# Kernel tuning notes

Measured on AMD Instinct MI355X. Metric: run time of the kernel, lower is better.

Reference implementation:

```python
import jax, jax.numpy as jnp
import numpy as np

B, N, DIN, D, E, STEP = 4, 1024, 256, 256, 5, 5


def setup_inputs() -> dict:
    key = jax.random.key(0)
    ks = jax.random.split(key, 14)
    s = 0.02  # weight init scale
    inp = {
        "node_features": jax.random.normal(ks[0], (B, N, DIN), dtype=jnp.float32),
        # dense per-edge-type adjacency; scaled so messages stay in a sane range
        "adj_matrices": jax.random.uniform(ks[1], (B, E, N, N), dtype=jnp.float32) * (2.0 / N),
        "fc_in_w": jax.random.normal(ks[2], (D, DIN), dtype=jnp.float32) * s,
        "fc_in_b": jnp.zeros((D,), dtype=jnp.float32),
        "edge_w": jax.random.normal(ks[3], (E, D, D), dtype=jnp.float32) * s,
        "edge_b": jax.random.normal(ks[4], (E, D), dtype=jnp.float32) * s,
        "gru_w_ih": jax.random.normal(ks[5], (3 * D, D), dtype=jnp.float32) * s,
        "gru_w_hh": jax.random.normal(ks[6], (3 * D, D), dtype=jnp.float32) * s,
        "gru_b_ih": jnp.zeros((3 * D,), dtype=jnp.float32),
        "gru_b_hh": jnp.zeros((3 * D,), dtype=jnp.float32),
        "conv1_w": jax.random.normal(ks[7], (D, D), dtype=jnp.float32) * s,
        "conv1_b": jnp.zeros((D,), dtype=jnp.float32),
        "conv2_w": jax.random.normal(ks[8], (D, D), dtype=jnp.float32) * s,
        "conv2_b": jnp.zeros((D,), dtype=jnp.float32),
    }
    return inp


def _gru_cell(x, h, w_ih, w_hh, b_ih, b_hh):
    # torch GRUCell: gates ordered [r, z, n]
    gi = x @ w_ih.T + b_ih  # [B*N, 3D]
    gh = h @ w_hh.T + b_hh
    ir, iz, inn = jnp.split(gi, 3, axis=-1)
    hr, hz, hn = jnp.split(gh, 3, axis=-1)
    r = jax.nn.sigmoid(ir + hr)
    z = jax.nn.sigmoid(iz + hz)
    n = jnp.tanh(inn + r * hn)
    return (1.0 - z) * n + z * h


def reference(node_features, adj_matrices, fc_in_w, fc_in_b, edge_w, edge_b,
              gru_w_ih, gru_w_hh, gru_b_ih, gru_b_hh,
              conv1_w, conv1_b, conv2_w, conv2_b):
    h = node_features @ fc_in_w.T + fc_in_b  # [B, N, D]
    sum_edge_b = jnp.sum(edge_b, axis=0)  # accumulated biases over edge types
    for _ in range(STEP):
        # messages per edge type: adj_e @ h  -> [B, E, N, D]
        msgs = jnp.einsum('benm,bmd->bend', adj_matrices, h)
        # per-edge-type linear (y = x @ W_e.T) then accumulate over edge types
        acc = jnp.einsum('bend,ekd->bnk', msgs, edge_w) + sum_edge_b  # [B, N, D]
        h = _gru_cell(acc, h, gru_w_ih, gru_w_hh, gru_b_ih, gru_b_hh)
    node_states = h  # [B, N, D]
    # conv1d with kernel_size=1 over node axis == per-node linear on channels
    attn_weights = jax.nn.sigmoid(node_states @ conv1_w.T + conv1_b)  # [B, N, D]
    feats = jnp.tanh(node_states @ conv2_w.T + conv2_b)  # [B, N, D]
    graph_embedding = jnp.sum(attn_weights * feats, axis=1)  # sum over nodes -> [B, D]
    attn_map = jnp.mean(attn_weights, axis=2)  # mean over channels -> [B, N]
    return (graph_embedding, node_states, attn_map)
```

## Files before the change

### kernel.cpp

```cpp
#include <hip/hip_runtime.h>
#include <hip/hip_bf16.h>
#include <cstdint>


typedef __attribute__((ext_vector_type(8))) short bf16x8;
typedef __attribute__((ext_vector_type(4))) float f32x4;

__device__ __forceinline__ float bf2f(__hip_bfloat16 x) { return __bfloat162float(x); }
__device__ __forceinline__ __hip_bfloat16 f2bf(float x) { return __float2bfloat16(x); }
__device__ __forceinline__ short f2bs(float x) {
  __hip_bfloat16 h = __float2bfloat16(x);
  return *reinterpret_cast<short*>(&h);
}
__device__ __forceinline__ float s2f(short x) {
  __hip_bfloat16 h = *reinterpret_cast<__hip_bfloat16*>(&x);
  return __bfloat162float(h);
}

__device__ __forceinline__ bf16x8 ld8_ext(const void* base, long off, bool f32) {
  if (f32) {
    const float* p = (const float*)base + off;
    bf16x8 r;
#pragma unroll
    for (int i = 0; i < 8; ++i) r[i] = f2bs(p[i]);
    return r;
  }
  return *(const bf16x8*)((const __hip_bfloat16*)base + off);
}

__device__ __forceinline__ bf16x8 ld8_sum5(const __hip_bfloat16* part, int row, int k) {
  const long base = (long)row * 256 + (long)(row >> 10) * 1048576 + k;
  float s[8] = {0.f, 0.f, 0.f, 0.f, 0.f, 0.f, 0.f, 0.f};
#pragma unroll
  for (int e = 0; e < 5; ++e) {
    bf16x8 v = *(const bf16x8*)(part + base + e * 262144);
#pragma unroll
    for (int j = 0; j < 8; ++j) s[j] += s2f(v[j]);
  }
  bf16x8 r;
#pragma unroll
  for (int j = 0; j < 8; ++j) r[j] = f2bs(s[j]);
  return r;
}

__device__ __forceinline__ void gload16(const __hip_bfloat16* g, __hip_bfloat16* l) {
  __builtin_amdgcn_global_load_lds(
      (const __attribute__((address_space(1))) void*)g,
      (__attribute__((address_space(3))) void*)l, 16, 0, 0);
}

__global__ void detect_dtype(const uint32_t* __restrict__ raw, int* __restrict__ flag) {
  __shared__ int cnt;
  if (threadIdx.x == 0) cnt = 0;
  __syncthreads();
  int c = 0;
  for (int i = threadIdx.x; i < 512; i += 256) {
    uint32_t byte = (raw[i] >> 8) & 0xFF;
    if (byte >= 0x28 && byte <= 0x40) ++c;
  }
  atomicAdd(&cnt, c);
  __syncthreads();
  if (threadIdx.x == 0) *flag = (cnt < 300) ? 1 : 0;
}

__global__ void prep_pool(const void* fcb, const void* bih, const void* bhh,
                          const void* c1b, const void* c2b, const void* edgeb,
                          const int* __restrict__ flag,
                          float* __restrict__ pool, float* __restrict__ ge,
                          float* __restrict__ am32) {
  const bool f32 = (*flag != 0);
  for (int t = threadIdx.x; t < 2560; t += 256) {
    const void* p; int i;
    if (t < 256)       { p = fcb;  i = t; }
    else if (t < 1024) { p = bih;  i = t - 256; }
    else if (t < 1792) { p = bhh;  i = t - 1024; }
    else if (t < 2048) { p = c1b;  i = t - 1792; }
    else if (t < 2304) { p = c2b;  i = t - 2048; }
    else {
      int k = t - 2304; float s = 0.f;
      for (int e = 0; e < 5; ++e)
        s += f32 ? ((const float*)edgeb)[e * 256 + k]
                 : bf2f(((const __hip_bfloat16*)edgeb)[e * 256 + k]);
      pool[t] = s; continue;
    }
    pool[t] = f32 ? ((const float*)p)[i] : bf2f(((const __hip_bfloat16*)p)[i]);
  }
  for (int t = threadIdx.x; t < 1024; t += 256) ge[t] = 0.f;
  for (int t = threadIdx.x; t < 4096; t += 256) am32[t] = 0.f;
}

__global__ void bias_gi_k(const float* __restrict__ pool,
                          const __hip_bfloat16* __restrict__ wih,
                          float* __restrict__ out) {
  const int n = blockIdx.x * 256 + threadIdx.x;
  if (n >= 768) return;
  float s = pool[256 + n];
  for (int k = 0; k < 256; ++k) s += pool[2304 + k] * bf2f(wih[n * 256 + k]);
  out[n] = s;
}

__global__ void wcvt_all(const void* fcw, const void* edw, const void* wih,
                         const void* whh, const void* c1w, const void* c2w,
                         const int* __restrict__ flag, __hip_bfloat16* __restrict__ dst) {
  const bool f32 = (*flag != 0);
  const int i = blockIdx.x * 256 + threadIdx.x;
  const void* src; int off;
  if      (i < 65536)  { src = fcw; off = i; }
  else if (i < 393216) { src = edw; off = i - 65536; }
  else if (i < 589824) { src = wih; off = i - 393216; }
  else if (i < 786432) { src = whh; off = i - 589824; }
  else if (i < 851968) { src = c1w; off = i - 786432; }
  else                 { src = c2w; off = i - 851968; }
  dst[i] = f32 ? f2bf(((const float*)src)[off])
               : ((const __hip_bfloat16*)src)[off];
}

__global__ void adj_cvt(const void* __restrict__ src, const int* __restrict__ flag,
                        __hip_bfloat16* __restrict__ dst) {
  const bool f32 = (*flag != 0);
  const long i = ((long)blockIdx.x * 256 + threadIdx.x) * 8;
  bf16x8 r;
  if (f32) {
    const float* p = (const float*)src + i;
#pragma unroll
    for (int j = 0; j < 8; ++j) r[j] = f2bs(p[j]);
  } else {
    r = *(const bf16x8*)((const __hip_bfloat16*)src + i);
  }
  *(bf16x8*)(dst + i) = r;
}

__global__ void sum_part(const __hip_bfloat16* __restrict__ part,
                         __hip_bfloat16* __restrict__ out) {
  const int t = blockIdx.x * 256 + threadIdx.x;
  const int row = t >> 5;
  const int k = (t & 31) * 8;
  const long base = (long)row * 256 + (long)(row >> 10) * 1048576 + k;
  float s[8] = {0.f, 0.f, 0.f, 0.f, 0.f, 0.f, 0.f, 0.f};
#pragma unroll
  for (int e = 0; e < 5; ++e) {
    bf16x8 v = *(const bf16x8*)(part + base + e * 262144);
#pragma unroll
    for (int j = 0; j < 8; ++j) s[j] += s2f(v[j]);
  }
  bf16x8 r;
#pragma unroll
  for (int j = 0; j < 8; ++j) r[j] = f2bs(s[j]);
  *(bf16x8*)(out + (long)row * 256 + k) = r;
}

template<bool HAS_BIAS, bool DUAL>
__global__ __launch_bounds__(256)
void gemm128(const __hip_bfloat16* __restrict__ A, const __hip_bfloat16* __restrict__ Bt,
             const float* __restrict__ bias, __hip_bfloat16* __restrict__ C,
             const __hip_bfloat16* __restrict__ A2, const __hip_bfloat16* __restrict__ Bt2,
             const float* __restrict__ bias2, __hip_bfloat16* __restrict__ C2,
             int K, int lda, int ldb, int ldc,
             long aBatch, int zdivA, int zmodA,
             long bBatch, int zdivB, int zmodB,
             long cBatch, int zdivC, int zSplit)
{
  __shared__ __align__(16) __hip_bfloat16 sA[128 * 64];
  __shared__ __align__(16) __hip_bfloat16 sB[128 * 64];
  const int t = threadIdx.x;
  const int w = t >> 6;
  const int l = t & 63;
  const int m0 = blockIdx.x * 128;
  const int n0 = blockIdx.y * 128;
  int z = blockIdx.z;

  const __hip_bfloat16* Au = A; const __hip_bfloat16* Btu = Bt;
  const float* biasu = bias; __hip_bfloat16* Cu = C;
  if (DUAL && z >= zSplit) { Au = A2; Btu = Bt2; biasu = bias2; Cu = C2; z -= zSplit; }

  const __hip_bfloat16* Ab = Au + (long)((z / zdivA) % zmodA) * aBatch;
  const __hip_bfloat16* Bb = Btu + (long)((z / zdivB) % zmodB) * bBatch;

  const int srow = l >> 3;
  const int scol = (l & 7) * 8;

  f32x4 acc[4][4];
#pragma unroll
  for (int i = 0; i < 4; ++i)
#pragma unroll
    for (int j = 0; j < 4; ++j) acc[i][j] = (f32x4){0.f, 0.f, 0.f, 0.f};

  const int wr = (w >> 1) * 64;
  const int wc = (w & 1) * 64;
  const int r15 = l & 15;
  const int quad = l >> 4;

  for (int k0 = 0; k0 < K; k0 += 64) {
    __syncthreads();
#pragma unroll
    for (int i = 0; i < 4; ++i) {
      const int c = w * 4 + i;
      const int row = c * 8 + srow;
      gload16(Ab + (long)(m0 + row) * lda + (k0 + scol), sA + c * 512);
      gload16(Bb + (long)(n0 + row) * ldb + (k0 + scol), sB + c * 512);
    }
    __syncthreads();
#pragma unroll
    for (int ks = 0; ks < 2; ++ks) {
      const int cg = (ks * 4 + quad) * 8;
      bf16x8 aF[4], bF[4];
#pragma unroll
      for (int i = 0; i < 4; ++i)
        aF[i] = *(const bf16x8*)(sA + (wr + i * 16 + r15) * 64 + cg);
#pragma unroll
      for (int i = 0; i < 4; ++i)
        bF[i] = *(const bf16x8*)(sB + (wc + i * 16 + r15) * 64 + cg);
#pragma unroll
      for (int mi = 0; mi < 4; ++mi)
#pragma unroll
        for (int ni = 0; ni < 4; ++ni)
          acc[mi][ni] = __builtin_amdgcn_mfma_f32_16x16x32_bf16(
              aF[mi], bF[ni], acc[mi][ni], 0, 0, 0);
    }
  }

  const long cOff = (long)(z / zdivC) * cBatch;
#pragma unroll
  for (int mi = 0; mi < 4; ++mi) {
#pragma unroll
    for (int ni = 0; ni < 4; ++ni) {
      const int n = n0 + wc + ni * 16 + r15;
      float bv = 0.f;
      if (HAS_BIAS) bv = biasu[n];
#pragma unroll
      for (int r = 0; r < 4; ++r) {
        const int m = m0 + wr + mi * 16 + quad * 4 + r;
        Cu[cOff + (long)m * ldc + n] = f2bf(acc[mi][ni][r] + bv);
      }
    }
  }
}

template<int OUT_MODE, bool HAS_BIAS, int A_MODE, bool DUAL>
__global__ __launch_bounds__(256)
void gemm_bt(const void* __restrict__ A, const __hip_bfloat16* __restrict__ Bt,
             const float* __restrict__ bias, void* __restrict__ Cp,
             const void* __restrict__ A2, const __hip_bfloat16* __restrict__ Bt2,
             const float* __restrict__ bias2, void* __restrict__ Cp2,
             const int* __restrict__ flag,
             int Kg, int ngrp, int lda, int ldb, int ldc,
             long aBatch, int zdivA, int zmodA,
             long bBatch, int zdivB, int zmodB,
             long cBatch, int zdivC, long aGrp, long bGrp, int zSplit)
{
  __shared__ __align__(16) __hip_bfloat16 sA[64 * 64];
  __shared__ __align__(16) __hip_bfloat16 sB[64 * 64];
  const bool af32 = (A_MODE == 1) ? (*flag != 0) : false;
  const int t = threadIdx.x;
  const int w = t >> 6;
  const int l = t & 63;
  const int m0 = blockIdx.x * 64;
  const int n0 = blockIdx.y * 64;
  int z = blockIdx.z;

  const void* Au = A; const __hip_bfloat16* Btu = Bt;
  const float* biasu = bias; void* Cpu = Cp;
  bool second = false;
  if (DUAL && z >= zSplit) {
    Au = A2; Btu = Bt2; biasu = bias2; Cpu = Cp2; z -= zSplit; second = true;
  }

  const long aOff = (long)((z / zdivA) % zmodA) * aBatch;
  const __hip_bfloat16* Bb = Btu + (long)((z / zdivB) % zmodB) * bBatch;

  const int p0 = t, p1 = t + 256;
  const int sr0 = p0 >> 3, sc0 = (p0 & 7) ^ (sr0 & 7);
  const int sr1 = p1 >> 3, sc1 = (p1 & 7) ^ (sr1 & 7);

  f32x4 acc[4];
#pragma unroll
  for (int i = 0; i < 4; ++i) acc[i] = (f32x4){0.f, 0.f, 0.f, 0.f};

  const int mrow = w * 16 + (l & 15);
  const int quad = l >> 4;

  for (int g = 0; g < ngrp; ++g) {
    const long aG = aOff + (long)g * aGrp;
    const __hip_bfloat16* Bg = Bb + (long)g * bGrp;
    for (int k0 = 0; k0 < Kg; k0 += 64) {
      bf16x8 a0, a1;
      if (A_MODE == 2 && !second) {
        a0 = ld8_sum5((const __hip_bfloat16*)Au, m0 + sr0, k0 + sc0 * 8);
        a1 = ld8_sum5((const __hip_bfloat16*)Au, m0 + sr1, k0 + sc1 * 8);
      } else if (A_MODE == 1) {
        a0 = ld8_ext(Au, aG + (long)(m0 + sr0) * lda + (k0 + sc0 * 8), af32);
        a1 = ld8_ext(Au, aG + (long)(m0 + sr1) * lda + (k0 + sc1 * 8), af32);
      } else {
        const __hip_bfloat16* Ab = (const __hip_bfloat16*)Au;
        a0 = *(const bf16x8*)(Ab + aG + (long)(m0 + sr0) * lda + (k0 + sc0 * 8));
        a1 = *(const bf16x8*)(Ab + aG + (long)(m0 + sr1) * lda + (k0 + sc1 * 8));
      }
      bf16x8 b0 = *(const bf16x8*)(Bg + (long)(n0 + sr0) * ldb + (k0 + sc0 * 8));
      bf16x8 b1 = *(const bf16x8*)(Bg + (long)(n0 + sr1) * ldb + (k0 + sc1 * 8));
      __syncthreads();
      *(bf16x8*)(sA + p0 * 8) = a0;
      *(bf16x8*)(sA + p1 * 8) = a1;
      *(bf16x8*)(sB + p0 * 8) = b0;
      *(bf16x8*)(sB + p1 * 8) = b1;
      __syncthreads();
#pragma unroll
      for (int ks = 0; ks < 2; ++ks) {
        const int cg = ks * 4 + quad;
        bf16x8 af = *(const bf16x8*)(sA + mrow * 64 + ((cg ^ (mrow & 7)) * 8));
#pragma unroll
        for (int t4 = 0; t4 < 4; ++t4) {
          const int nrow = t4 * 16 + (l & 15);
          bf16x8 bfr = *(const bf16x8*)(sB + nrow * 64 + ((cg ^ (nrow & 7)) * 8));
          acc[t4] = __builtin_amdgcn_mfma_f32_16x16x32_bf16(af, bfr, acc[t4], 0, 0, 0);
        }
      }
    }
  }

  const long cOff = (long)(z / zdivC) * cBatch;
#pragma unroll
  for (int t4 = 0; t4 < 4; ++t4) {
    const int n = n0 + t4 * 16 + (l & 15);
    float bv = 0.f;
    if (HAS_BIAS) bv = biasu[n];
#pragma unroll
    for (int r = 0; r < 4; ++r) {
      const int m = m0 + w * 16 + quad * 4 + r;
      const float v = acc[t4][r] + bv;
      if (OUT_MODE == 0)
        ((__hip_bfloat16*)Cpu)[cOff + (long)m * ldc + n] = f2bf(v);
      else
        ((float*)Cpu)[cOff + (long)m * ldc + n] = v;
    }
  }
}

__global__ void gru_gate8(const __hip_bfloat16* __restrict__ gi,
                          const __hip_bfloat16* __restrict__ gh,
                          __hip_bfloat16* __restrict__ hbf,
                          void* __restrict__ ns_out, const int* __restrict__ flag)
{
  const int t = blockIdx.x * 256 + threadIdx.x;
  const int m = t >> 5;
  const int k = (t & 31) * 8;
  const long gb = (long)m * 768 + k;
  bf16x8 vir = *(const bf16x8*)(gi + gb);
  bf16x8 viz = *(const bf16x8*)(gi + gb + 256);
  bf16x8 vin = *(const bf16x8*)(gi + gb + 512);
  bf16x8 vhr = *(const bf16x8*)(gh + gb);
  bf16x8 vhz = *(const bf16x8*)(gh + gb + 256);
  bf16x8 vhn = *(const bf16x8*)(gh + gb + 512);
  const long hidx = (long)m * 256 + k;
  bf16x8 vh = *(const bf16x8*)(hbf + hidx);
  bf16x8 out;
  float hf[8];
#pragma unroll
  for (int j = 0; j < 8; ++j) {
    const float r = 1.f / (1.f + __expf(-(s2f(vir[j]) + s2f(vhr[j]))));
    const float zz = 1.f / (1.f + __expf(-(s2f(viz[j]) + s2f(vhz[j]))));
    const float nn = tanhf(s2f(vin[j]) + r * s2f(vhn[j]));
    hf[j] = (1.f - zz) * nn + zz * s2f(vh[j]);
    out[j] = f2bs(hf[j]);
  }
  *(bf16x8*)(hbf + hidx) = out;
  if (ns_out) {
    if (*flag) {
      float* o = (float*)ns_out + 1024 + hidx;
#pragma unroll
      for (int j = 0; j < 8; ++j) o[j] = hf[j];
    } else {
      *(bf16x8*)((__hip_bfloat16*)ns_out + 1024 + hidx) = out;
    }
  }
}

__global__ __launch_bounds__(256)
void conv_fused(const __hip_bfloat16* __restrict__ hbf,
                const __hip_bfloat16* __restrict__ c1w,
                const __hip_bfloat16* __restrict__ c2w,
                const float* __restrict__ pool,
                float* __restrict__ geg, float* __restrict__ am32)
{
  __shared__ __align__(16) __hip_bfloat16 sA[64 * 64];
  __shared__ __align__(16) __hip_bfloat16 sB1[64 * 64];
  __shared__ __align__(16) __hip_bfloat16 sB2[64 * 64];
  __shared__ float sge[64];
  __shared__ float sam[64];
  const int t = threadIdx.x, w = t >> 6, l = t & 63;
  const int m0 = blockIdx.x * 64, n0 = blockIdx.y * 64;
  if (t < 64) { sge[t] = 0.f; sam[t] = 0.f; }
  const int p0 = t, p1 = t + 256;
  const int sr0 = p0 >> 3, sc0 = (p0 & 7) ^ (sr0 & 7);
  const int sr1 = p1 >> 3, sc1 = (p1 & 7) ^ (sr1 & 7);
  f32x4 a1[4], a2[4];
#pragma unroll
  for (int i = 0; i < 4; ++i) { a1[i] = (f32x4){0,0,0,0}; a2[i] = (f32x4){0,0,0,0}; }
  const int mrow = w * 16 + (l & 15);
  const int quad = l >> 4;
  for (int k0 = 0; k0 < 256; k0 += 64) {
    bf16x8 va0 = *(const bf16x8*)(hbf + (long)(m0 + sr0) * 256 + (k0 + sc0 * 8));
    bf16x8 va1 = *(const bf16x8*)(hbf + (long)(m0 + sr1) * 256 + (k0 + sc1 * 8));
    bf16x8 vb0 = *(const bf16x8*)(c1w + (long)(n0 + sr0) * 256 + (k0 + sc0 * 8));
    bf16x8 vb1 = *(const bf16x8*)(c1w + (long)(n0 + sr1) * 256 + (k0 + sc1 * 8));
    bf16x8 vc0 = *(const bf16x8*)(c2w + (long)(n0 + sr0) * 256 + (k0 + sc0 * 8));
    bf16x8 vc1 = *(const bf16x8*)(c2w + (long)(n0 + sr1) * 256 + (k0 + sc1 * 8));
    __syncthreads();
    *(bf16x8*)(sA + p0 * 8) = va0;  *(bf16x8*)(sA + p1 * 8) = va1;
    *(bf16x8*)(sB1 + p0 * 8) = vb0; *(bf16x8*)(sB1 + p1 * 8) = vb1;
    *(bf16x8*)(sB2 + p0 * 8) = vc0; *(bf16x8*)(sB2 + p1 * 8) = vc1;
    __syncthreads();
#pragma unroll
    for (int ks = 0; ks < 2; ++ks) {
      const int cg = ks * 4 + quad;
      bf16x8 af = *(const bf16x8*)(sA + mrow * 64 + ((cg ^ (mrow & 7)) * 8));
#pragma unroll
      for (int t4 = 0; t4 < 4; ++t4) {
        const int nrow = t4 * 16 + (l & 15);
        bf16x8 b1f = *(const bf16x8*)(sB1 + nrow * 64 + ((cg ^ (nrow & 7)) * 8));
        bf16x8 b2f = *(const bf16x8*)(sB2 + nrow * 64 + ((cg ^ (nrow & 7)) * 8));
        a1[t4] = __builtin_amdgcn_mfma_f32_16x16x32_bf16(af, b1f, a1[t4], 0, 0, 0);
        a2[t4] = __builtin_amdgcn_mfma_f32_16x16x32_bf16(af, b2f, a2[t4], 0, 0, 0);
      }
    }
  }
  float asum[4] = {0.f, 0.f, 0.f, 0.f};
#pragma unroll
  for (int t4 = 0; t4 < 4; ++t4) {
    const int n = n0 + t4 * 16 + (l & 15);
    const float bb1 = pool[1792 + n], bb2 = pool[2048 + n];
    float g = 0.f;
#pragma unroll
    for (int r = 0; r < 4; ++r) {
      const float av = 1.f / (1.f + __expf(-(a1[t4][r] + bb1)));
      const float fv = tanhf(a2[t4][r] + bb2);
      g += av * fv;
      asum[r] += av;
    }
    atomicAdd(&sge[t4 * 16 + (l & 15)], g);
  }
#pragma unroll
  for (int r = 0; r < 4; ++r) atomicAdd(&sam[w * 16 + quad * 4 + r], asum[r]);
  __syncthreads();
  if (t < 64) atomicAdd(&geg[(m0 >> 10) * 256 + n0 + t], sge[t]);
  else if (t < 128) atomicAdd(&am32[m0 + (t - 64)], sam[t - 64]);
}

__global__ void finish_out(const float* __restrict__ ge, const float* __restrict__ am32,
                           void* __restrict__ dout, const int* __restrict__ flag)
{
  const int t = blockIdx.x * 256 + threadIdx.x;
  const bool f32 = (*flag != 0);
  if (t < 1024) {
    if (f32) ((float*)dout)[t] = ge[t];
    else     ((__hip_bfloat16*)dout)[t] = f2bf(ge[t]);
  } else {
    const float v = am32[t - 1024] * (1.f / 256.f);
    if (f32) ((float*)dout)[1049600 + t - 1024] = v;
    else     ((__hip_bfloat16*)dout)[1049600 + t - 1024] = f2bf(v);
  }
}

extern "C" void kernel_launch(void* const* d_in, const int* in_sizes, int n_in,
                              void* d_out, int out_size, void* d_ws, size_t ws_size,
                              hipStream_t stream) {
  (void)in_sizes; (void)n_in; (void)out_size;
  const void* node_f = d_in[0];
  const void* adj    = d_in[1];
  const void* fc_w   = d_in[2];
  const void* fc_b   = d_in[3];
  const void* edge_w = d_in[4];
  const void* edge_b = d_in[5];
  const void* w_ih   = d_in[6];
  const void* w_hh   = d_in[7];
  const void* b_ih   = d_in[8];
  const void* b_hh   = d_in[9];
  const void* c1w    = d_in[10];
  const void* c1b    = d_in[11];
  const void* c2w    = d_in[12];
  const void* c2b    = d_in[13];

  char* ws = (char*)d_ws;
  const size_t MB = (size_t)1 << 20;
  int*            flag = (int*)(ws);
  float*          bp   = (float*)(ws + 256);
  float*          ge   = (float*)(ws + 14336);
  float*          am32 = (float*)(ws + 18432);
  __hip_bfloat16* wbf  = (__hip_bfloat16*)(ws + 34816);
  __hip_bfloat16* hbf  = (__hip_bfloat16*)(ws + 1869824);
  char*           S    = ws + 3966976;
  __hip_bfloat16* heT  = (__hip_bfloat16*)(S);
  __hip_bfloat16* part = (__hip_bfloat16*)(S + 10 * MB);
  __hip_bfloat16* gi   = (__hip_bfloat16*)(S + 20 * MB);
  __hip_bfloat16* gh   = (__hip_bfloat16*)(S + 26 * MB);
  __hip_bfloat16* spt  = (__hip_bfloat16*)(S + 32 * MB);
  __hip_bfloat16* adjb = (__hip_bfloat16*)(ws + 40 * MB);

  const bool has_split = ws_size >= 38 * MB;
  const bool has_adjb  = ws_size >= 81 * MB;

  detect_dtype<<<1, 256, 0, stream>>>((const uint32_t*)adj, flag);
  prep_pool<<<1, 256, 0, stream>>>(fc_b, b_ih, b_hh, c1b, c2b, edge_b, flag, bp, ge, am32);
  wcvt_all<<<3584, 256, 0, stream>>>(fc_w, edge_w, w_ih, w_hh, c1w, c2w, flag, wbf);
  bias_gi_k<<<3, 256, 0, stream>>>(bp, wbf + 393216, bp + 2560);
  if (has_adjb) adj_cvt<<<10240, 256, 0, stream>>>(adj, flag, adjb);

  gemm_bt<0, true, 1, false><<<dim3(64, 4, 1), 256, 0, stream>>>(
      node_f, wbf + 0, bp + 0, hbf, nullptr, nullptr, nullptr, nullptr, flag,
      256, 1, 256, 256, 256, 0, 1, 1, 0, 1, 1, 0, 1, 0, 0, 0);

  for (int s = 0; s < 5; ++s) {
    if (has_adjb) {
      gemm128<false, false><<<dim3(2, 8, 20), 256, 0, stream>>>(
          wbf + 65536, hbf, nullptr, heT, nullptr, nullptr, nullptr, nullptr,
          256, 256, 256, 1024,
          65536, 1, 5,
          262144, 5, 4,
          262144, 1, 0);
      gemm128<false, false><<<dim3(8, 2, 20), 256, 0, stream>>>(
          adjb, heT, nullptr, part, nullptr, nullptr, nullptr, nullptr,
          1024, 1024, 1024, 256,
          1048576, 1, 20,
          262144, 1, 20,
          262144, 1, 0);
      sum_part<<<512, 256, 0, stream>>>(part, spt);
      gemm128<true, true><<<dim3(32, 6, 2), 256, 0, stream>>>(
          spt, wbf + 393216, bp + 2560, gi,
          hbf, wbf + 589824, bp + 1024, gh,
          256, 256, 256, 768,
          0, 1, 1, 0, 1, 1, 0, 1, 1);
    } else if (has_split) {
      gemm_bt<0, false, 0, false><<<dim3(4, 16, 20), 256, 0, stream>>>(
          wbf + 65536, hbf, nullptr, heT, nullptr, nullptr, nullptr, nullptr, flag,
          256, 1, 256, 256, 1024,
          65536, 1, 5, 262144, 5, 4,
          262144, 1, 0, 0, 0);
      gemm_bt<0, false, 1, false><<<dim3(16, 4, 20), 256, 0, stream>>>(
          adj, heT, nullptr, part, nullptr, nullptr, nullptr, nullptr, flag,
          1024, 1, 1024, 1024, 256,
          1048576, 1, 20, 262144, 1, 20,
          262144, 1, 0, 0, 0);
      gemm_bt<0, true, 2, true><<<dim3(64, 12, 2), 256, 0, stream>>>(
          part, wbf + 393216, bp + 2560, gi,
          hbf,  wbf + 589824, bp + 1024, gh, flag,
          256, 1, 256, 256, 768, 0, 1, 1, 0, 1, 1, 0, 1, 0, 0, 1);
    } else {
      gemm_bt<0, false, 0, false><<<dim3(4, 16, 20), 256, 0, stream>>>(
          wbf + 65536, hbf, nullptr, heT, nullptr, nullptr, nullptr, nullptr, flag,
          256, 1, 256, 256, 1024,
          65536, 1, 5, 262144, 5, 4,
          262144, 1, 0, 0, 0);
      gemm_bt<0, true, 1, false><<<dim3(16, 4, 4), 256, 0, stream>>>(
          adj, heT, bp + 2304, part, nullptr, nullptr, nullptr, nullptr, flag,
          1024, 5, 1024, 1024, 256,
          (long)5 * 1048576, 1, 4, (long)5 * 262144, 1, 4,
          262144, 1, 1048576, 262144, 0);
      gemm_bt<0, true, 0, true><<<dim3(64, 12, 2), 256, 0, stream>>>(
          part, wbf + 393216, bp + 256, gi,
          hbf,  wbf + 589824, bp + 1024, gh, flag,
          256, 1, 256, 256, 768, 0, 1, 1, 0, 1, 1, 0, 1, 0, 0, 1);
    }
    gru_gate8<<<512, 256, 0, stream>>>(gi, gh, hbf,
                                       (s == 4) ? d_out : nullptr, flag);
  }

  conv_fused<<<dim3(64, 4), 256, 0, stream>>>(hbf, wbf + 786432, wbf + 851968,
                                              bp, ge, am32);
  finish_out<<<20, 256, 0, stream>>>(ge, am32, d_out, flag);
}
```

Before: 500.1 us.

## Switch GEMM tile to 128x64 with register-staged XOR-swizzled LDS loads

Changes the main bf16 GEMM tile from 128x128 to 128x64 and doubles the grid's N dimension, giving each wave a 32x64 output slice. Tiles now go global to registers to LDS with an XOR swizzle on 16-byte chunks, replacing the direct global_load_lds path, to avoid LDS bank conflicts on fragment reads and put more blocks in flight on small grids. The cost is lower operand reuse per block, more blocks, and a register staging step.

```diff
diff --git a/kernel.cpp b/kernel.cpp
--- a/kernel.cpp
+++ b/kernel.cpp
@@ -41,12 +41,6 @@
 #pragma unroll
   for (int j = 0; j < 8; ++j) r[j] = f2bs(s[j]);
   return r;
-}
-
-__device__ __forceinline__ void gload16(const __hip_bfloat16* g, __hip_bfloat16* l) {
-  __builtin_amdgcn_global_load_lds(
-      (const __attribute__((address_space(1))) void*)g,
-      (__attribute__((address_space(3))) void*)l, 16, 0, 0);
 }
 
 __global__ void detect_dtype(const uint32_t* __restrict__ raw, int* __restrict__ flag) {
@@ -151,22 +145,22 @@
 
 template<bool HAS_BIAS, bool DUAL>
 __global__ __launch_bounds__(256)
-void gemm128(const __hip_bfloat16* __restrict__ A, const __hip_bfloat16* __restrict__ Bt,
-             const float* __restrict__ bias, __hip_bfloat16* __restrict__ C,
-             const __hip_bfloat16* __restrict__ A2, const __hip_bfloat16* __restrict__ Bt2,
-             const float* __restrict__ bias2, __hip_bfloat16* __restrict__ C2,
-             int K, int lda, int ldb, int ldc,
-             long aBatch, int zdivA, int zmodA,
-             long bBatch, int zdivB, int zmodB,
-             long cBatch, int zdivC, int zSplit)
+void gemm_bt128(const __hip_bfloat16* __restrict__ A, const __hip_bfloat16* __restrict__ Bt,
+                const float* __restrict__ bias, __hip_bfloat16* __restrict__ C,
+                const __hip_bfloat16* __restrict__ A2, const __hip_bfloat16* __restrict__ Bt2,
+                const float* __restrict__ bias2, __hip_bfloat16* __restrict__ C2,
+                int K, int lda, int ldb, int ldc,
+                long aBatch, int zdivA, int zmodA,
+                long bBatch, int zdivB, int zmodB,
+                long cBatch, int zdivC, int zSplit)
 {
   __shared__ __align__(16) __hip_bfloat16 sA[128 * 64];
-  __shared__ __align__(16) __hip_bfloat16 sB[128 * 64];
+  __shared__ __align__(16) __hip_bfloat16 sB[64 * 64];
   const int t = threadIdx.x;
   const int w = t >> 6;
   const int l = t & 63;
   const int m0 = blockIdx.x * 128;
-  const int n0 = blockIdx.y * 128;
+  const int n0 = blockIdx.y * 64;
   int z = blockIdx.z;
 
   const __hip_bfloat16* Au = A; const __hip_bfloat16* Btu = Bt;
@@ -176,42 +170,55 @@
   const __hip_bfloat16* Ab = Au + (long)((z / zdivA) % zmodA) * aBatch;
   const __hip_bfloat16* Bb = Btu + (long)((z / zdivB) % zmodB) * bBatch;
 
-  const int srow = l >> 3;
-  const int scol = (l & 7) * 8;
-
-  f32x4 acc[4][4];
-#pragma unroll
-  for (int i = 0; i < 4; ++i)
+  int sra[4], sca[4];
+#pragma unroll
+  for (int i = 0; i < 4; ++i) {
+    const int p = t + 256 * i;
+    sra[i] = p >> 3;
+    sca[i] = (p & 7) ^ (sra[i] & 7);
+  }
+  const int p0 = t, p1 = t + 256;
+  const int sr0 = p0 >> 3, sc0 = (p0 & 7) ^ (sr0 & 7);
+  const int sr1 = p1 >> 3, sc1 = (p1 & 7) ^ (sr1 & 7);
+
+  f32x4 acc[2][4];
+#pragma unroll
+  for (int i = 0; i < 2; ++i)
 #pragma unroll
     for (int j = 0; j < 4; ++j) acc[i][j] = (f32x4){0.f, 0.f, 0.f, 0.f};
 
-  const int wr = (w >> 1) * 64;
-  const int wc = (w & 1) * 64;
   const int r15 = l & 15;
   const int quad = l >> 4;
 
   for (int k0 = 0; k0 < K; k0 += 64) {
+    bf16x8 av[4];
+#pragma unroll
+    for (int i = 0; i < 4; ++i)
+      av[i] = *(const bf16x8*)(Ab + (long)(m0 + sra[i]) * lda + (k0 + sca[i] * 8));
+    bf16x8 b0 = *(const bf16x8*)(Bb + (long)(n0 + sr0) * ldb + (k0 + sc0 * 8));
+    bf16x8 b1 = *(const bf16x8*)(Bb + (long)(n0 + sr1) * ldb + (k0 + sc1 * 8));
     __syncthreads();
 #pragma unroll
-    for (int i = 0; i < 4; ++i) {
-      const int c = w * 4 + i;
-      const int row = c * 8 + srow;
-      gload16(Ab + (long)(m0 + row) * lda + (k0 + scol), sA + c * 512);
-      gload16(Bb + (long)(n0 + row) * ldb + (k0 + scol), sB + c * 512);
-    }
+    for (int i = 0; i < 4; ++i) *(bf16x8*)(sA + (t + 256 * i) * 8) = av[i];
+    *(bf16x8*)(sB + p0 * 8) = b0;
+    *(bf16x8*)(sB + p1 * 8) = b1;
     __syncthreads();
 #pragma unroll
     for (int ks = 0; ks < 2; ++ks) {
-      const int cg = (ks * 4 + quad) * 8;
-      bf16x8 aF[4], bF[4];
-#pragma unroll
-      for (int i = 0; i < 4; ++i)
-        aF[i] = *(const bf16x8*)(sA + (wr + i * 16 + r15) * 64 + cg);
-#pragma unroll
-      for (int i = 0; i < 4; ++i)
-        bF[i] = *(const bf16x8*)(sB + (wc + i * 16 + r15) * 64 + cg);
-#pragma unroll
-      for (int mi = 0; mi < 4; ++mi)
+      const int cg = ks * 4 + quad;
+      bf16x8 aF[2], bF[4];
+#pragma unroll
+      for (int mi = 0; mi < 2; ++mi) {
+        const int row = mi * 64 + w * 16 + r15;
+        aF[mi] = *(const bf16x8*)(sA + row * 64 + ((cg ^ (row & 7)) * 8));
+      }
+#pragma unroll
+      for (int ni = 0; ni < 4; ++ni) {
+        const int nrow = ni * 16 + r15;
+        bF[ni] = *(const bf16x8*)(sB + nrow * 64 + ((cg ^ (nrow & 7)) * 8));
+      }
+#pragma unroll
+      for (int mi = 0; mi < 2; ++mi)
 #pragma unroll
         for (int ni = 0; ni < 4; ++ni)
           acc[mi][ni] = __builtin_amdgcn_mfma_f32_16x16x32_bf16(
@@ -221,15 +228,15 @@
 
   const long cOff = (long)(z / zdivC) * cBatch;
 #pragma unroll
-  for (int mi = 0; mi < 4; ++mi) {
+  for (int mi = 0; mi < 2; ++mi) {
 #pragma unroll
     for (int ni = 0; ni < 4; ++ni) {
-      const int n = n0 + wc + ni * 16 + r15;
+      const int n = n0 + ni * 16 + r15;
       float bv = 0.f;
       if (HAS_BIAS) bv = biasu[n];
 #pragma unroll
       for (int r = 0; r < 4; ++r) {
-        const int m = m0 + wr + mi * 16 + quad * 4 + r;
+        const int m = m0 + mi * 64 + w * 16 + quad * 4 + r;
         Cu[cOff + (long)m * ldc + n] = f2bf(acc[mi][ni][r] + bv);
       }
     }
@@ -510,20 +517,20 @@
 
   for (int s = 0; s < 5; ++s) {
     if (has_adjb) {
-      gemm128<false, false><<<dim3(2, 8, 20), 256, 0, stream>>>(
+      gemm_bt128<false, false><<<dim3(2, 16, 20), 256, 0, stream>>>(
           wbf + 65536, hbf, nullptr, heT, nullptr, nullptr, nullptr, nullptr,
           256, 256, 256, 1024,
           65536, 1, 5,
           262144, 5, 4,
           262144, 1, 0);
-      gemm128<false, false><<<dim3(8, 2, 20), 256, 0, stream>>>(
+      gemm_bt128<false, false><<<dim3(8, 4, 20), 256, 0, stream>>>(
           adjb, heT, nullptr, part, nullptr, nullptr, nullptr, nullptr,
           1024, 1024, 1024, 256,
           1048576, 1, 20,
           262144, 1, 20,
           262144, 1, 0);
       sum_part<<<512, 256, 0, stream>>>(part, spt);
-      gemm128<true, true><<<dim3(32, 6, 2), 256, 0, stream>>>(
+      gemm_bt128<true, true><<<dim3(32, 12, 2), 256, 0, stream>>>(
           spt, wbf + 393216, bp + 2560, gi,
           hbf, wbf + 589824, bp + 1024, gh,
           256, 256, 256, 768,
```

New measurement: 449.3 us. 10.1% less time.
